# Kernel tuning notes

Measured on AMD Instinct MI355X. Metric: run time of the kernel, lower is better.

The kernel has to match this reference:

```python
import jax, jax.numpy as jnp
import numpy as np

B, S, D, H = 4, 1024, 1024, 16
DH = D // H  # 64


def setup_inputs() -> dict:
    key = jax.random.key(0)
    ks = jax.random.split(key, 6)
    x = jax.random.normal(ks[0], (B, S, D), dtype=jnp.float32)
    y = jax.random.normal(ks[1], (B, S, D), dtype=jnp.float32)
    z = jax.random.normal(ks[2], (B, S, D), dtype=jnp.float32)
    key_padding_mask = jnp.zeros((B, S), dtype=bool)
    # Linear weights, torch layout [out_features, in_features], fan-in scaled
    W_qkv = jax.random.normal(ks[3], (3 * D, D), dtype=jnp.float32) / np.sqrt(D)
    W_proj = jax.random.normal(ks[4], (D, D), dtype=jnp.float32) / np.sqrt(D)
    b_proj = jnp.zeros((D,), dtype=jnp.float32)
    return {"x": x, "y": y, "z": z, "key_padding_mask": key_padding_mask,
            "W_qkv": W_qkv, "W_proj": W_proj, "b_proj": b_proj}


def reference(x, y, z, key_padding_mask, W_qkv, W_proj, b_proj):
    # y, z, key_padding_mask are unused in the original forward.
    b, s, d = x.shape
    qkv = jnp.einsum('bsd,ed->bse', x, W_qkv)                  # [B,S,3D]
    qkv = qkv.reshape(b, s, 3, H, DH)
    q, k, v = (qkv[:, :, i].transpose(0, 2, 1, 3) for i in range(3))  # [B,H,S,DH]
    scores = jnp.einsum('bhqd,bhkd->bhqk', q, k)               # [B,H,S,S]
    causal = jnp.triu(jnp.ones((s, s), dtype=bool), k=1)       # True above diag
    scores = jnp.where(causal, -jnp.inf, scores)
    # NOTE: faithful to source bug: scores / d_head**(-0.5) == scores * sqrt(d_head)
    attn_weights = jax.nn.softmax(scores * jnp.sqrt(jnp.float32(DH)), axis=-1)
    # dropout p=0.0 (eval): identity
    ctx = jnp.einsum('bhqk,bhkd->bhqd', attn_weights, v)       # [B,H,S,DH]
    ctx = ctx.transpose(0, 2, 1, 3).reshape(b, s, d)           # [B,S,D]
    out = jnp.einsum('bsd,ed->bse', ctx, W_proj) + b_proj
    return out, attn_weights
```

## Files before the change

### kernel.cpp

```cpp
#include <hip/hip_runtime.h>
#include <hip/hip_bf16.h>

typedef __bf16 bf16_t;
typedef __bf16 bf16x8 __attribute__((ext_vector_type(8)));
typedef __bf16 bf16x4 __attribute__((ext_vector_type(4)));
typedef float f32x4 __attribute__((ext_vector_type(4)));
typedef unsigned int u32;

#define MFMA16 __builtin_amdgcn_mfma_f32_16x16x32_bf16
static constexpr float MASKV = -1.0e30f;
static constexpr int Sdim = 1024;

__device__ __forceinline__ void gload16(const void* g, void* l) {
    __builtin_amdgcn_global_load_lds((const __attribute__((address_space(1))) u32*)g,
                                     (__attribute__((address_space(3))) u32*)l, 16, 0, 0);
}

__device__ __forceinline__ void splt2(float v, bf16_t* h, bf16_t* l) {
    const bf16_t hv = (bf16_t)v;
    *h = hv; *l = (bf16_t)(v - (float)hv);
}

static constexpr int QX = 1048576;
static constexpr int QW = 786432;

__global__ __launch_bounds__(256) void split2_k(
    const float* __restrict__ x, const float* __restrict__ wqkv, const float* __restrict__ wproj,
    bf16_t* __restrict__ xh, bf16_t* __restrict__ xl,
    bf16_t* __restrict__ wh, bf16_t* __restrict__ wl, bf16_t* __restrict__ wp)
{
    int q = blockIdx.x * 256 + threadIdx.x;
    const int stride = 2048 * 256;
#pragma unroll
    for (int it = 0; it < 4; ++it, q += stride) {
        if (q < QX + QW) {
            const float* src; bf16_t *dh, *dl;
            if (q < QX) { src = x + (size_t)q * 4; dh = xh + (size_t)q * 4; dl = xl + (size_t)q * 4; }
            else { const int r = q - QX; src = wqkv + (size_t)r * 4; dh = wh + (size_t)r * 4; dl = wl + (size_t)r * 4; }
            const f32x4 v = *(const f32x4*)src;
            bf16x4 hv, lv;
#pragma unroll
            for (int c = 0; c < 4; ++c) { bf16_t a, b; splt2(v[c], &a, &b); hv[c] = a; lv[c] = b; }
            *(bf16x4*)dh = hv; *(bf16x4*)dl = lv;
        } else {
            const int r = q - QX - QW;
            const f32x4 v = *(const f32x4*)(wproj + (size_t)r * 4);
            bf16x4 hv;
#pragma unroll
            for (int c = 0; c < 4; ++c) hv[c] = (bf16_t)v[c];
            *(bf16x4*)(wp + (size_t)r * 4) = hv;
        }
    }
}

__global__ __launch_bounds__(256) void gemm_qkv(
    const bf16_t* __restrict__ Ah_g, const bf16_t* __restrict__ Al_g,
    const bf16_t* __restrict__ Bh_g, const bf16_t* __restrict__ Bl_g,
    float* __restrict__ Qf, float* __restrict__ Kf, bf16_t* __restrict__ Vt)
{
    __shared__ bf16_t Ah[128 * 32], Al[128 * 32], Bh[128 * 32], Bl[128 * 32];
    const int tid = threadIdx.x, w = tid >> 6, lane = tid & 63;
    const int lm = lane & 15, hi = lane >> 4;
    const int wr = w >> 1, wc = w & 1;
    const int m0 = blockIdx.x * 128, n0 = blockIdx.y * 128;
    const int isel = n0 >> 10;
    const bool three = (isel < 2);

    f32x4 acc[4][4] = {};

    for (int kt = 0; kt < 32; ++kt) {
        __syncthreads();
#pragma unroll
        for (int c = 0; c < 2; ++c) {
            const int j = c * 256 + tid;
            const int r = j >> 2, cg = (j & 3) << 3;
            const int base = (c * 256 + w * 64) * 8;
            const size_t goa = (size_t)(m0 + r) * 1024 + kt * 32 + cg;
            const size_t gob = (size_t)(n0 + r) * 1024 + kt * 32 + cg;
            gload16(Ah_g + goa, &Ah[base]);
            gload16(Bh_g + gob, &Bh[base]);
            if (three) {
                gload16(Al_g + goa, &Al[base]);
                gload16(Bl_g + gob, &Bl[base]);
            }
        }
        __syncthreads();

        bf16x8 ah[4], bh[4], al[4], bl[4];
#pragma unroll
        for (int mi = 0; mi < 4; ++mi)
            ah[mi] = *(const bf16x8*)&Ah[(wr * 64 + mi * 16 + lm) * 32 + hi * 8];
#pragma unroll
        for (int ni = 0; ni < 4; ++ni)
            bh[ni] = *(const bf16x8*)&Bh[(wc * 64 + ni * 16 + lm) * 32 + hi * 8];
        if (three) {
#pragma unroll
            for (int mi = 0; mi < 4; ++mi)
                al[mi] = *(const bf16x8*)&Al[(wr * 64 + mi * 16 + lm) * 32 + hi * 8];
#pragma unroll
            for (int ni = 0; ni < 4; ++ni)
                bl[ni] = *(const bf16x8*)&Bl[(wc * 64 + ni * 16 + lm) * 32 + hi * 8];
        }
#pragma unroll
        for (int mi = 0; mi < 4; ++mi)
#pragma unroll
            for (int ni = 0; ni < 4; ++ni) {
                if (three) {
                    acc[mi][ni] = MFMA16(ah[mi], bl[ni], acc[mi][ni], 0, 0, 0);
                    acc[mi][ni] = MFMA16(al[mi], bh[ni], acc[mi][ni], 0, 0, 0);
                }
                acc[mi][ni] = MFMA16(ah[mi], bh[ni], acc[mi][ni], 0, 0, 0);
            }
    }

#pragma unroll
    for (int mi = 0; mi < 4; ++mi)
#pragma unroll
        for (int ni = 0; ni < 4; ++ni)
#pragma unroll
            for (int j = 0; j < 4; ++j) {
                const float v = acc[mi][ni][j];
                const int m = m0 + wr * 64 + mi * 16 + hi * 4 + j;
                const int e = n0 + wc * 64 + ni * 16 + lm;
                const int b = m >> 10, s = m & 1023;
                const int h = (e >> 6) & 15, dh = e & 63;
                if (isel == 0)
                    Qf[(((size_t)(b * 16 + h)) * Sdim + s) * 64 + dh] = v;
                else if (isel == 1)
                    Kf[(((size_t)(b * 16 + h)) * Sdim + s) * 64 + dh] = v;
                else
                    Vt[(((size_t)(b * 16 + h)) * 64 + dh) * Sdim + s] = (bf16_t)v;
            }
}

__global__ __launch_bounds__(256) void attn_k(
    const float* __restrict__ Qf, const float* __restrict__ Kf,
    const bf16_t* __restrict__ Vt, float* __restrict__ attnW, bf16_t* __restrict__ ctx)
{
    constexpr int PITCH = 1036;
    __shared__ float S[16][PITCH];
    const int qt = blockIdx.x, bh = blockIdx.y;
    const int q0 = qt * 16;
    const int tid = threadIdx.x, w = tid >> 6, lane = tid & 63;
    const int lm = lane & 15, hi = lane >> 4;
    const int KT = qt + 1, KT16 = KT * 16;

    const float* qp = Qf + ((size_t)bh * Sdim + q0 + lm) * 64 + hi * 8;
    bf16x8 qh0, ql0, qh1, ql1;
    {
        const f32x4 a0 = *(const f32x4*)qp,        a1 = *(const f32x4*)(qp + 4);
        const f32x4 b0 = *(const f32x4*)(qp + 32), b1 = *(const f32x4*)(qp + 36);
#pragma unroll
        for (int i = 0; i < 4; ++i) {
            bf16_t h, l;
            splt2(a0[i], &h, &l); qh0[i] = h;   ql0[i] = l;
            splt2(a1[i], &h, &l); qh0[i+4] = h; ql0[i+4] = l;
            splt2(b0[i], &h, &l); qh1[i] = h;   ql1[i] = l;
            splt2(b1[i], &h, &l); qh1[i+4] = h; ql1[i+4] = l;
        }
    }

    for (int kt = w; kt < KT; kt += 4) {
        const float* kp = Kf + ((size_t)bh * Sdim + kt * 16 + lm) * 64 + hi * 8;
        bf16x8 kh0, kl0, kh1, kl1;
        {
            const f32x4 a0 = *(const f32x4*)kp,        a1 = *(const f32x4*)(kp + 4);
            const f32x4 b0 = *(const f32x4*)(kp + 32), b1 = *(const f32x4*)(kp + 36);
#pragma unroll
            for (int i = 0; i < 4; ++i) {
                bf16_t h, l;
                splt2(a0[i], &h, &l); kh0[i] = h;   kl0[i] = l;
                splt2(a1[i], &h, &l); kh0[i+4] = h; kl0[i+4] = l;
                splt2(b0[i], &h, &l); kh1[i] = h;   kl1[i] = l;
                splt2(b1[i], &h, &l); kh1[i+4] = h; kl1[i+4] = l;
            }
        }
        f32x4 t = {0.f, 0.f, 0.f, 0.f};
        t = MFMA16(ql0, kh0, t, 0, 0, 0);
        t = MFMA16(ql1, kh1, t, 0, 0, 0);
        t = MFMA16(qh0, kl0, t, 0, 0, 0);
        t = MFMA16(qh1, kl1, t, 0, 0, 0);
        t = MFMA16(qh0, kh0, t, 0, 0, 0);
        t = MFMA16(qh1, kh1, t, 0, 0, 0);
        const int c = kt * 16 + lm;
#pragma unroll
        for (int j = 0; j < 4; ++j) {
            const int r = hi * 4 + j;
            S[r][c] = (c <= q0 + r) ? t[j] * 8.0f : MASKV;
        }
    }
    __syncthreads();

#pragma unroll
    for (int rr = 0; rr < 4; ++rr) {
        const int r = w * 4 + rr;
        float mx = MASKV;
        for (int cb = 0; cb < Sdim; cb += 256) {
            if (cb >= KT16) break;
            const int c = cb + lane * 4;
            const f32x4 v = *(const f32x4*)&S[r][c];
#pragma unroll
            for (int cc = 0; cc < 4; ++cc)
                if (c + cc < KT16) mx = fmaxf(mx, v[cc]);
        }
#pragma unroll
        for (int dd = 1; dd < 64; dd <<= 1) mx = fmaxf(mx, __shfl_xor(mx, dd));

        float z = 0.f;
        for (int cb = 0; cb < Sdim; cb += 256) {
            const int c = cb + lane * 4;
            const f32x4 v = *(const f32x4*)&S[r][c];
            f32x4 e;
#pragma unroll
            for (int cc = 0; cc < 4; ++cc) {
                const float a = fmaxf(v[cc] - mx, -87.0f);
                const float ev = (c + cc < KT16) ? __expf(a) : 0.f;
                e[cc] = ev; z += ev;
            }
            *(f32x4*)&S[r][c] = e;
        }
#pragma unroll
        for (int dd = 1; dd < 64; dd <<= 1) z += __shfl_xor(z, dd);
        const float invZ = 1.0f / z;

        float* arow = attnW + ((size_t)bh * Sdim + q0 + r) * Sdim;
        for (int cb = 0; cb < Sdim; cb += 256) {
            const int c = cb + lane * 4;
            const f32x4 e = *(const f32x4*)&S[r][c];
            f32x4 p;
#pragma unroll
            for (int cc = 0; cc < 4; ++cc) p[cc] = e[cc] * invZ;
            *(f32x4*)&S[r][c] = p;
            *(f32x4*)(arow + c) = p;
        }
    }
    __syncthreads();

    f32x4 acc = {0.f, 0.f, 0.f, 0.f};
    const int steps = (KT16 + 31) >> 5;
    const bf16_t* vtp = Vt + ((size_t)bh * 64 + w * 16 + lm) * Sdim;
    for (int ks = 0; ks < steps; ++ks) {
        const int kb = ks * 32 + hi * 8;
        const f32x4 v0 = *(const f32x4*)&S[lm][kb];
        const f32x4 v1 = *(const f32x4*)&S[lm][kb + 4];
        bf16x8 a;
#pragma unroll
        for (int i = 0; i < 4; ++i) { a[i] = (bf16_t)v0[i]; a[i + 4] = (bf16_t)v1[i]; }
        const bf16x8 bfr = *(const bf16x8*)(vtp + kb);
        acc = MFMA16(a, bfr, acc, 0, 0, 0);
    }
    const int bb = bh >> 4, h = bh & 15;
#pragma unroll
    for (int j = 0; j < 4; ++j) {
        const int s = q0 + hi * 4 + j;
        ctx[((size_t)bb * Sdim + s) * 1024 + h * 64 + w * 16 + lm] = (bf16_t)acc[j];
    }
}

__global__ __launch_bounds__(256) void gemm_proj(
    const bf16_t* __restrict__ A, const bf16_t* __restrict__ Bw,
    const float* __restrict__ bias, float* __restrict__ out)
{
    __shared__ bf16_t As[128 * 32];
    __shared__ bf16_t Bs[128 * 32];
    const int tid = threadIdx.x, w = tid >> 6, lane = tid & 63;
    const int lm = lane & 15, hi = lane >> 4;
    const int wr = w >> 1, wc = w & 1;
    const int m0 = blockIdx.x * 128, n0 = blockIdx.y * 128;

    f32x4 acc[4][4] = {};
    for (int kt = 0; kt < 32; ++kt) {
        __syncthreads();
#pragma unroll
        for (int c = 0; c < 2; ++c) {
            const int j = c * 256 + tid;
            const int r = j >> 2, cg = (j & 3) << 3;
            const int base = (c * 256 + w * 64) * 8;
            gload16(A  + (size_t)(m0 + r) * 1024 + kt * 32 + cg, &As[base]);
            gload16(Bw + (size_t)(n0 + r) * 1024 + kt * 32 + cg, &Bs[base]);
        }
        __syncthreads();
        bf16x8 af[4], bfr[4];
#pragma unroll
        for (int mi = 0; mi < 4; ++mi)
            af[mi] = *(const bf16x8*)&As[(wr * 64 + mi * 16 + lm) * 32 + hi * 8];
#pragma unroll
        for (int ni = 0; ni < 4; ++ni)
            bfr[ni] = *(const bf16x8*)&Bs[(wc * 64 + ni * 16 + lm) * 32 + hi * 8];
#pragma unroll
        for (int mi = 0; mi < 4; ++mi)
#pragma unroll
            for (int ni = 0; ni < 4; ++ni)
                acc[mi][ni] = MFMA16(af[mi], bfr[ni], acc[mi][ni], 0, 0, 0);
    }
#pragma unroll
    for (int mi = 0; mi < 4; ++mi)
#pragma unroll
        for (int ni = 0; ni < 4; ++ni) {
            const int e = n0 + wc * 64 + ni * 16 + lm;
            const float bv = bias[e];
#pragma unroll
            for (int j = 0; j < 4; ++j) {
                const int m = m0 + wr * 64 + mi * 16 + hi * 4 + j;
                out[(size_t)m * 1024 + e] = acc[mi][ni][j] + bv;
            }
        }
}

extern "C" void kernel_launch(void* const* d_in, const int* in_sizes, int n_in,
                              void* d_out, int out_size, void* d_ws, size_t ws_size,
                              hipStream_t stream)
{
    const float* big[3] = {nullptr, nullptr, nullptr}; int nbig = 0;
    const float* Wqkv = nullptr; const float* Wproj = nullptr; const float* bproj = nullptr;
    for (int i = 0; i < n_in; ++i) {
        const int sz = in_sizes[i];
        if (sz == 4194304)      { if (nbig < 3) big[nbig++] = (const float*)d_in[i]; }
        else if (sz == 3145728) { Wqkv  = (const float*)d_in[i]; }
        else if (sz == 1048576) { Wproj = (const float*)d_in[i]; }
        else if (sz == 1024)    { bproj = (const float*)d_in[i]; }
    }
    const float* x = big[0];

    float* out   = (float*)d_out;
    float* attnW = out + (size_t)4194304;

    bf16_t* xh = (bf16_t*)attnW;
    bf16_t* xl = xh + (size_t)4194304;
    bf16_t* wh = xl + (size_t)4194304;
    bf16_t* wl = wh + (size_t)3145728;

    char* wsb = (char*)d_ws;
    float*  Qf  = (float*)wsb;
    float*  Kf  = (float*)(wsb + ((size_t)16 << 20));
    bf16_t* Vt  = (bf16_t*)(wsb + ((size_t)32 << 20));
    bf16_t* ctx = (bf16_t*)(wsb + ((size_t)40 << 20));
    bf16_t* wp  = (bf16_t*)(wsb + ((size_t)48 << 20));

    split2_k<<<2048, 256, 0, stream>>>(x, Wqkv, Wproj, xh, xl, wh, wl, wp);
    gemm_qkv<<<dim3(32, 24), 256, 0, stream>>>(xh, xl, wh, wl, Qf, Kf, Vt);
    attn_k<<<dim3(64, 64), 256, 0, stream>>>(Qf, Kf, Vt, attnW, ctx);
    gemm_proj<<<dim3(32, 8), 256, 0, stream>>>(ctx, wp, bproj, out);
}
```

Baseline: 271.1 us.

## Pre-split Q/K into bf16 hi/lo in QKV GEMM, reorder attention blocks, unroll loops

The QKV GEMM epilogue now writes Q and K as separate bf16 high and low planes instead of fp32, so the attention kernel loads ready MFMA operands and no longer redoes the split per key tile. The attention grid is reordered so the heaviest causal query tiles launch first, to reduce tail imbalance. The QK^T loop processes two key tiles per iteration and the PV loop uses two accumulators, which adds independent MFMA chains for better latency hiding. This costs more registers and a slightly more complex epilogue with scattered bf16 stores.

Result: faster. 253.2 us (-6.6%).

```diff
diff --git a/kernel.cpp b/kernel.cpp
--- a/kernel.cpp
+++ b/kernel.cpp
@@ -56,7 +56,8 @@
 __global__ __launch_bounds__(256) void gemm_qkv(
     const bf16_t* __restrict__ Ah_g, const bf16_t* __restrict__ Al_g,
     const bf16_t* __restrict__ Bh_g, const bf16_t* __restrict__ Bl_g,
-    float* __restrict__ Qf, float* __restrict__ Kf, bf16_t* __restrict__ Vt)
+    bf16_t* __restrict__ Qhi, bf16_t* __restrict__ Qlo,
+    bf16_t* __restrict__ Khi, bf16_t* __restrict__ Klo, bf16_t* __restrict__ Vt)
 {
     __shared__ bf16_t Ah[128 * 32], Al[128 * 32], Bh[128 * 32], Bl[128 * 32];
     const int tid = threadIdx.x, w = tid >> 6, lane = tid & 63;
@@ -124,69 +125,82 @@
                 const int e = n0 + wc * 64 + ni * 16 + lm;
                 const int b = m >> 10, s = m & 1023;
                 const int h = (e >> 6) & 15, dh = e & 63;
-                if (isel == 0)
-                    Qf[(((size_t)(b * 16 + h)) * Sdim + s) * 64 + dh] = v;
-                else if (isel == 1)
-                    Kf[(((size_t)(b * 16 + h)) * Sdim + s) * 64 + dh] = v;
-                else
+                if (isel < 2) {
+                    const size_t off = (((size_t)(b * 16 + h)) * Sdim + s) * 64 + dh;
+                    bf16_t hv, lv; splt2(v, &hv, &lv);
+                    if (isel == 0) { Qhi[off] = hv; Qlo[off] = lv; }
+                    else           { Khi[off] = hv; Klo[off] = lv; }
+                } else {
                     Vt[(((size_t)(b * 16 + h)) * 64 + dh) * Sdim + s] = (bf16_t)v;
+                }
             }
 }
 
 __global__ __launch_bounds__(256) void attn_k(
-    const float* __restrict__ Qf, const float* __restrict__ Kf,
+    const bf16_t* __restrict__ Qhi, const bf16_t* __restrict__ Qlo,
+    const bf16_t* __restrict__ Khi, const bf16_t* __restrict__ Klo,
     const bf16_t* __restrict__ Vt, float* __restrict__ attnW, bf16_t* __restrict__ ctx)
 {
     constexpr int PITCH = 1036;
     __shared__ float S[16][PITCH];
-    const int qt = blockIdx.x, bh = blockIdx.y;
+    const int bh = blockIdx.x;
+    const int qt = 63 - blockIdx.y;
     const int q0 = qt * 16;
     const int tid = threadIdx.x, w = tid >> 6, lane = tid & 63;
     const int lm = lane & 15, hi = lane >> 4;
     const int KT = qt + 1, KT16 = KT * 16;
 
-    const float* qp = Qf + ((size_t)bh * Sdim + q0 + lm) * 64 + hi * 8;
-    bf16x8 qh0, ql0, qh1, ql1;
-    {
-        const f32x4 a0 = *(const f32x4*)qp,        a1 = *(const f32x4*)(qp + 4);
-        const f32x4 b0 = *(const f32x4*)(qp + 32), b1 = *(const f32x4*)(qp + 36);
-#pragma unroll
-        for (int i = 0; i < 4; ++i) {
-            bf16_t h, l;
-            splt2(a0[i], &h, &l); qh0[i] = h;   ql0[i] = l;
-            splt2(a1[i], &h, &l); qh0[i+4] = h; ql0[i+4] = l;
-            splt2(b0[i], &h, &l); qh1[i] = h;   ql1[i] = l;
-            splt2(b1[i], &h, &l); qh1[i+4] = h; ql1[i+4] = l;
-        }
-    }
-
-    for (int kt = w; kt < KT; kt += 4) {
-        const float* kp = Kf + ((size_t)bh * Sdim + kt * 16 + lm) * 64 + hi * 8;
-        bf16x8 kh0, kl0, kh1, kl1;
-        {
-            const f32x4 a0 = *(const f32x4*)kp,        a1 = *(const f32x4*)(kp + 4);
-            const f32x4 b0 = *(const f32x4*)(kp + 32), b1 = *(const f32x4*)(kp + 36);
-#pragma unroll
-            for (int i = 0; i < 4; ++i) {
-                bf16_t h, l;
-                splt2(a0[i], &h, &l); kh0[i] = h;   kl0[i] = l;
-                splt2(a1[i], &h, &l); kh0[i+4] = h; kl0[i+4] = l;
-                splt2(b0[i], &h, &l); kh1[i] = h;   kl1[i] = l;
-                splt2(b1[i], &h, &l); kh1[i+4] = h; kl1[i+4] = l;
-            }
-        }
-        f32x4 t = {0.f, 0.f, 0.f, 0.f};
-        t = MFMA16(ql0, kh0, t, 0, 0, 0);
-        t = MFMA16(ql1, kh1, t, 0, 0, 0);
-        t = MFMA16(qh0, kl0, t, 0, 0, 0);
-        t = MFMA16(qh1, kl1, t, 0, 0, 0);
-        t = MFMA16(qh0, kh0, t, 0, 0, 0);
-        t = MFMA16(qh1, kh1, t, 0, 0, 0);
-        const int c = kt * 16 + lm;
+    const size_t qoff = ((size_t)bh * Sdim + q0 + lm) * 64 + hi * 8;
+    const bf16x8 qh0 = *(const bf16x8*)(Qhi + qoff);
+    const bf16x8 qh1 = *(const bf16x8*)(Qhi + qoff + 32);
+    const bf16x8 ql0 = *(const bf16x8*)(Qlo + qoff);
+    const bf16x8 ql1 = *(const bf16x8*)(Qlo + qoff + 32);
+
+    const bf16_t* Khb = Khi + (size_t)bh * Sdim * 64;
+    const bf16_t* Klb = Klo + (size_t)bh * Sdim * 64;
+
+    for (int kt = w; kt < KT; kt += 8) {
+        const size_t o1 = (size_t)(kt * 16 + lm) * 64 + hi * 8;
+        const bf16x8 kh0a = *(const bf16x8*)(Khb + o1);
+        const bf16x8 kh1a = *(const bf16x8*)(Khb + o1 + 32);
+        const bf16x8 kl0a = *(const bf16x8*)(Klb + o1);
+        const bf16x8 kl1a = *(const bf16x8*)(Klb + o1 + 32);
+        const int kt2 = kt + 4;
+        const bool has2 = (kt2 < KT);
+        bf16x8 kh0b = kh0a, kh1b = kh1a, kl0b = kl0a, kl1b = kl1a;
+        if (has2) {
+            const size_t o2 = (size_t)(kt2 * 16 + lm) * 64 + hi * 8;
+            kh0b = *(const bf16x8*)(Khb + o2);
+            kh1b = *(const bf16x8*)(Khb + o2 + 32);
+            kl0b = *(const bf16x8*)(Klb + o2);
+            kl1b = *(const bf16x8*)(Klb + o2 + 32);
+        }
+        f32x4 t0 = {0.f, 0.f, 0.f, 0.f}, t1 = {0.f, 0.f, 0.f, 0.f};
+        t0 = MFMA16(ql0, kh0a, t0, 0, 0, 0);
+        t1 = MFMA16(ql0, kh0b, t1, 0, 0, 0);
+        t0 = MFMA16(ql1, kh1a, t0, 0, 0, 0);
+        t1 = MFMA16(ql1, kh1b, t1, 0, 0, 0);
+        t0 = MFMA16(qh0, kl0a, t0, 0, 0, 0);
+        t1 = MFMA16(qh0, kl0b, t1, 0, 0, 0);
+        t0 = MFMA16(qh1, kl1a, t0, 0, 0, 0);
+        t1 = MFMA16(qh1, kl1b, t1, 0, 0, 0);
+        t0 = MFMA16(qh0, kh0a, t0, 0, 0, 0);
+        t1 = MFMA16(qh0, kh0b, t1, 0, 0, 0);
+        t0 = MFMA16(qh1, kh1a, t0, 0, 0, 0);
+        t1 = MFMA16(qh1, kh1b, t1, 0, 0, 0);
+        const int c1 = kt * 16 + lm;
 #pragma unroll
         for (int j = 0; j < 4; ++j) {
             const int r = hi * 4 + j;
-            S[r][c] = (c <= q0 + r) ? t[j] * 8.0f : MASKV;
+            S[r][c1] = (c1 <= q0 + r) ? t0[j] * 8.0f : MASKV;
+        }
+        if (has2) {
+            const int c2 = kt2 * 16 + lm;
+#pragma unroll
+            for (int j = 0; j < 4; ++j) {
+                const int r = hi * 4 + j;
+                S[r][c2] = (c2 <= q0 + r) ? t1[j] * 8.0f : MASKV;
+            }
         }
     }
     __syncthreads();
@@ -236,19 +250,30 @@
     }
     __syncthreads();
 
-    f32x4 acc = {0.f, 0.f, 0.f, 0.f};
+    f32x4 acc0 = {0.f, 0.f, 0.f, 0.f}, acc1 = {0.f, 0.f, 0.f, 0.f};
     const int steps = (KT16 + 31) >> 5;
     const bf16_t* vtp = Vt + ((size_t)bh * 64 + w * 16 + lm) * Sdim;
-    for (int ks = 0; ks < steps; ++ks) {
-        const int kb = ks * 32 + hi * 8;
-        const f32x4 v0 = *(const f32x4*)&S[lm][kb];
-        const f32x4 v1 = *(const f32x4*)&S[lm][kb + 4];
-        bf16x8 a;
-#pragma unroll
-        for (int i = 0; i < 4; ++i) { a[i] = (bf16_t)v0[i]; a[i + 4] = (bf16_t)v1[i]; }
-        const bf16x8 bfr = *(const bf16x8*)(vtp + kb);
-        acc = MFMA16(a, bfr, acc, 0, 0, 0);
-    }
+    for (int ks = 0; ks < steps; ks += 2) {
+        {
+            const int kb = ks * 32 + hi * 8;
+            const f32x4 v0 = *(const f32x4*)&S[lm][kb];
+            const f32x4 v1 = *(const f32x4*)&S[lm][kb + 4];
+            bf16x8 a;
+#pragma unroll
+            for (int i = 0; i < 4; ++i) { a[i] = (bf16_t)v0[i]; a[i + 4] = (bf16_t)v1[i]; }
+            acc0 = MFMA16(a, *(const bf16x8*)(vtp + kb), acc0, 0, 0, 0);
+        }
+        if (ks + 1 < steps) {
+            const int kb = (ks + 1) * 32 + hi * 8;
+            const f32x4 v0 = *(const f32x4*)&S[lm][kb];
+            const f32x4 v1 = *(const f32x4*)&S[lm][kb + 4];
+            bf16x8 a;
+#pragma unroll
+            for (int i = 0; i < 4; ++i) { a[i] = (bf16_t)v0[i]; a[i + 4] = (bf16_t)v1[i]; }
+            acc1 = MFMA16(a, *(const bf16x8*)(vtp + kb), acc1, 0, 0, 0);
+        }
+    }
+    const f32x4 acc = acc0 + acc1;
     const int bb = bh >> 4, h = bh & 15;
 #pragma unroll
     for (int j = 0; j < 4; ++j) {
@@ -331,14 +356,16 @@
     bf16_t* wl = wh + (size_t)3145728;
 
     char* wsb = (char*)d_ws;
-    float*  Qf  = (float*)wsb;
-    float*  Kf  = (float*)(wsb + ((size_t)16 << 20));
+    bf16_t* Qhi = (bf16_t*)wsb;
+    bf16_t* Qlo = (bf16_t*)(wsb + ((size_t)8  << 20));
+    bf16_t* Khi = (bf16_t*)(wsb + ((size_t)16 << 20));
+    bf16_t* Klo = (bf16_t*)(wsb + ((size_t)24 << 20));
     bf16_t* Vt  = (bf16_t*)(wsb + ((size_t)32 << 20));
     bf16_t* ctx = (bf16_t*)(wsb + ((size_t)40 << 20));
     bf16_t* wp  = (bf16_t*)(wsb + ((size_t)48 << 20));
 
     split2_k<<<2048, 256, 0, stream>>>(x, Wqkv, Wproj, xh, xl, wh, wl, wp);
-    gemm_qkv<<<dim3(32, 24), 256, 0, stream>>>(xh, xl, wh, wl, Qf, Kf, Vt);
-    attn_k<<<dim3(64, 64), 256, 0, stream>>>(Qf, Kf, Vt, attnW, ctx);
+    gemm_qkv<<<dim3(32, 24), 256, 0, stream>>>(xh, xl, wh, wl, Qhi, Qlo, Khi, Klo, Vt);
+    attn_k<<<dim3(64, 64), 256, 0, stream>>>(Qhi, Qlo, Khi, Klo, Vt, attnW, ctx);
     gemm_proj<<<dim3(32, 8), 256, 0, stream>>>(ctx, wp, bproj, out);
 }
```
